# Performance work log

Hardware: AMD Instinct MI355X
Metric: run time of the kernel (lower is better)

## Reference

```python
import jax, jax.numpy as jnp
import numpy as np

D_MODEL = 1024
N_HEADS = 16
D_HEAD = D_MODEL // N_HEADS

def setup_inputs() -> dict:
    key = jax.random.key(0)
    k1, k2, k3 = jax.random.split(key, 3)
    x = jax.random.normal(k1, (4, 2048, D_MODEL), dtype=jnp.float32)
    # Linear weights stored as [in, out] for x @ W
    s = 1.0 / np.sqrt(D_MODEL)
    W_qkv = jax.random.uniform(k2, (D_MODEL, 3 * D_MODEL), jnp.float32, -s, s)
    W_out = jax.random.uniform(k3, (D_MODEL, D_MODEL), jnp.float32, -s, s)
    return {"x": x, "W_qkv": W_qkv, "W_out": W_out}

def reference(x, W_qkv, W_out):
    B, T, C = x.shape
    scale = D_HEAD ** -0.5
    qkv = x @ W_qkv                       # [B,T,3C]
    q, k, v = jnp.split(qkv, 3, axis=-1)
    def heads(t):
        return t.reshape(B, T, N_HEADS, D_HEAD).transpose(0, 2, 1, 3)  # [B,H,T,d]
    q, k, v = heads(q), heads(k), heads(v)
    att = jnp.einsum('bhqd,bhkd->bhqk', q, k) * scale  # [B,H,T,T]
    causal = jnp.tril(jnp.ones((T, T), dtype=bool))
    att = jnp.where(causal, att, -jnp.inf)
    att = jax.nn.softmax(att, axis=-1)
    y = jnp.einsum('bhqk,bhkd->bhqd', att, v)          # [B,H,T,d]
    y = y.transpose(0, 2, 1, 3).reshape(B, T, C)
    return y @ W_out
```

## Files before the change

kernel.cpp:

```cpp
#include <hip/hip_runtime.h>
#include <hip/hip_bf16.h>

typedef unsigned short u16;
typedef __attribute__((ext_vector_type(8))) short short8v;
typedef __attribute__((ext_vector_type(4))) float f32x4;
typedef __attribute__((ext_vector_type(16))) float f32x16;

#define Bb 4
#define Tt 2048
#define Cc 1024
#define Hh 16
#define C3 3072
#define Mm 8192

__device__ __forceinline__ u16 f2bf(float f) {
    union { __hip_bfloat16 h; u16 u; } r;
    r.h = __float2bfloat16(f);
    return r.u;
}
__device__ __forceinline__ unsigned int pk2(float a, float b) {
    union { __hip_bfloat162 h; unsigned int u; } r;
    r.h.x = __float2bfloat16(a);
    r.h.y = __float2bfloat16(b);
    return r.u;
}
__device__ __forceinline__ float exp2g(float x) {
#if __has_builtin(__builtin_amdgcn_exp2f)
    return __builtin_amdgcn_exp2f(x);
#else
    return exp2f(x);
#endif
}
__device__ __forceinline__ void plswap(unsigned int& a, unsigned int& b) {
#if __has_builtin(__builtin_amdgcn_permlane32_swap)
    typedef __attribute__((ext_vector_type(2))) unsigned int uint2v;
    uint2v r = __builtin_amdgcn_permlane32_swap(a, b, false, false);
    a = r.x; b = r.y;
#else
    asm volatile("v_permlane32_swap_b32 %0, %1" : "+v"(a), "+v"(b));
#endif
}
__device__ __forceinline__ void gload16(const void* g, void* l) {
    __builtin_amdgcn_global_load_lds(
        (const __attribute__((address_space(1))) unsigned int*)g,
        (__attribute__((address_space(3))) unsigned int*)l, 16, 0, 0);
}
__device__ __forceinline__ short8v scale8(short8v v, float s) {
    union { short8v sv; unsigned int u[4]; } in, out;
    in.sv = v;
#pragma unroll
    for (int i = 0; i < 4; ++i) {
        float lo = __uint_as_float(in.u[i] << 16);
        float hi = __uint_as_float(in.u[i] & 0xffff0000u);
        out.u[i] = pk2(lo * s, hi * s);
    }
    return out.sv;
}

__global__ __launch_bounds__(256) void cvt_x(const float* __restrict__ in,
                                             u16* __restrict__ out) {
    int i = blockIdx.x * 256 + threadIdx.x;
    float4 v = reinterpret_cast<const float4*>(in)[i];
    ushort4 o;
    o.x = f2bf(v.x); o.y = f2bf(v.y); o.z = f2bf(v.z); o.w = f2bf(v.w);
    reinterpret_cast<ushort4*>(out)[i] = o;
}

__global__ __launch_bounds__(256) void wtrans(const float* __restrict__ in,
                                              u16* __restrict__ out,
                                              int R, int Ccols) {
    __shared__ float t[32][33];
    const int tx = threadIdx.x & 31, ty = threadIdx.x >> 5;
    const int bx = blockIdx.x, by = blockIdx.y;
    const int c = bx * 32 + tx;
#pragma unroll
    for (int j = 0; j < 4; ++j) {
        int r = by * 32 + ty + j * 8;
        t[ty + j * 8][tx] = in[(size_t)r * Ccols + c];
    }
    __syncthreads();
#pragma unroll
    for (int j = 0; j < 4; ++j) {
        int orow = bx * 32 + ty + j * 8;
        int oc   = by * 32 + tx;
        out[(size_t)orow * R + oc] = f2bf(t[tx][ty + j * 8]);
    }
}

template <int OUTF32>
__global__ __launch_bounds__(256) void gemm_mfma(const u16* __restrict__ A,
                                                 const u16* __restrict__ BT,
                                                 void* __restrict__ C0,
                                                 int M, int N, int K) {
    __shared__ u16 As[128 * 32];
    __shared__ u16 Bs[128 * 32];
    const int tid = threadIdx.x;
    const int w = tid >> 6, l = tid & 63;
    const int wr = w >> 1, wc = w & 1;
    const int g = l >> 4, q = l & 15;
    const int bm = blockIdx.x * 128, bn = blockIdx.y * 128;
    const int lrow = l >> 2;
    const int lcol = (l & 3) * 8;

    f32x4 acc[4][4] = {};
    const u16* Ap = A + (size_t)(bm + w * 32 + lrow) * K + lcol;
    const u16* Bp = BT + (size_t)(bn + w * 32 + lrow) * K + lcol;

    for (int k0 = 0; k0 < K; k0 += 32) {
        gload16(Ap + k0, &As[(w * 32) * 32]);
        gload16(Ap + (size_t)16 * K + k0, &As[(w * 32 + 16) * 32]);
        gload16(Bp + k0, &Bs[(w * 32) * 32]);
        gload16(Bp + (size_t)16 * K + k0, &Bs[(w * 32 + 16) * 32]);
        __syncthreads();
        short8v af[4], bf[4];
#pragma unroll
        for (int m = 0; m < 4; ++m)
            af[m] = *reinterpret_cast<const short8v*>(&As[(wr * 64 + m * 16 + q) * 32 + g * 8]);
#pragma unroll
        for (int n = 0; n < 4; ++n)
            bf[n] = *reinterpret_cast<const short8v*>(&Bs[(wc * 64 + n * 16 + q) * 32 + g * 8]);
#pragma unroll
        for (int m = 0; m < 4; ++m)
#pragma unroll
            for (int n = 0; n < 4; ++n)
                acc[m][n] = __builtin_amdgcn_mfma_f32_16x16x32_bf16(af[m], bf[n], acc[m][n], 0, 0, 0);
        __syncthreads();
    }

#pragma unroll
    for (int m = 0; m < 4; ++m)
#pragma unroll
        for (int n = 0; n < 4; ++n)
#pragma unroll
            for (int r = 0; r < 4; ++r) {
                int row = bm + wr * 64 + m * 16 + g * 4 + r;
                int col = bn + wc * 64 + n * 16 + q;
                if (OUTF32)
                    reinterpret_cast<float*>(C0)[(size_t)row * N + col] = acc[m][n][r];
                else
                    reinterpret_cast<u16*>(C0)[(size_t)row * N + col] = f2bf(acc[m][n][r]);
            }
}

__global__ __launch_bounds__(512, 2) void gemm256_qkv(const u16* __restrict__ A,
                                                      const u16* __restrict__ BT,
                                                      u16* __restrict__ qkOut,
                                                      u16* __restrict__ vTOut,
                                                      int K) {
    __shared__ u16 SM[65536];
    const int tid = threadIdx.x;
    const int wv = tid >> 6, L = tid & 63;
    const int wm = wv >> 2, wn = wv & 3;
    const int q = L & 15, g = L >> 4;
    const int bm = blockIdx.x * 256, bn = blockIdx.y * 256;
    const int nK = K >> 6;

    char* smB = (char*)SM;
    const int srow = wv * 16 + (L >> 3);
    const int scol = ((L & 7) ^ ((L >> 3) & 7)) * 8;
    const u16* Asrc = A + (size_t)(bm + srow) * K + scol;
    const u16* Bsrc = BT + (size_t)(bn + srow) * K + scol;

#define STG2(src, ldsByte)                                                \
    { gload16((src), smB + (ldsByte) + wv * 2048);                        \
      gload16((src) + 8 * (size_t)K, smB + (ldsByte) + wv * 2048 + 1024); }

    STG2(Asrc, 0)
    STG2(Asrc + 128 * (size_t)K, 16384)
    STG2(Bsrc, 32768)
    STG2(Bsrc + 128 * (size_t)K, 49152)
    STG2(Asrc + 64, 65536)
    STG2(Asrc + 128 * (size_t)K + 64, 65536 + 16384)
    STG2(Bsrc + 64, 65536 + 32768)

    const int rA = (wm * 128 + q) * 64;
    const int rB = 16384 + (wn * 64 + q) * 64;
    const int s0 = (g ^ (q & 7)) * 8;
    const int s1 = ((4 + g) ^ (q & 7)) * 8;

    f32x4 acc[8][4] = {};

#define LDA2(dst, mf)                                                                   \
    dst[0] = *reinterpret_cast<const short8v*>(&SM[bufU + rA + mf * 1024 + s0]);        \
    dst[1] = *reinterpret_cast<const short8v*>(&SM[bufU + rA + mf * 1024 + s1]);
#define LDB2(nf)                                                                        \
    Bf##nf[0] = *reinterpret_cast<const short8v*>(&SM[bufU + rB + nf * 1024 + s0]);     \
    Bf##nf[1] = *reinterpret_cast<const short8v*>(&SM[bufU + rB + nf * 1024 + s1]);
#define MMA2(Aa, nf, ia)                                                                       \
    acc[ia][nf] = __builtin_amdgcn_mfma_f32_16x16x32_bf16(Aa[0], Bf##nf[0], acc[ia][nf], 0, 0, 0); \
    acc[ia][nf] = __builtin_amdgcn_mfma_f32_16x16x32_bf16(Aa[1], Bf##nf[1], acc[ia][nf], 0, 0, 0);
#define MBLK2(Aa, Ab, ia, ib)                                             \
    __builtin_amdgcn_s_setprio(1);                                        \
    MMA2(Aa, 0, ia) MMA2(Aa, 1, ia) MMA2(Aa, 2, ia) MMA2(Aa, 3, ia)       \
    MMA2(Ab, 0, ib) MMA2(Ab, 1, ib) MMA2(Ab, 2, ib) MMA2(Ab, 3, ib)       \
    __builtin_amdgcn_s_setprio(0);

    for (int t = 0; t < nK; ++t) {
        const int bufU = (t & 1) * 32768;
        const int curB = (t & 1) * 65536;
        const int nxtB = ((t + 1) & 1) * 65536;
        if (t == nK - 1) { asm volatile("s_waitcnt vmcnt(0)" ::: "memory"); }
        else             { asm volatile("s_waitcnt vmcnt(6)" ::: "memory"); }
        __builtin_amdgcn_s_barrier();
        __builtin_amdgcn_sched_barrier(0);

        short8v Bf0[2], Bf1[2], Bf2[2], Bf3[2];
        LDB2(0) LDB2(1) LDB2(2) LDB2(3)
        short8v Af0[2], Af1[2];
        LDA2(Af0, 0) LDA2(Af1, 1)
        if (t + 1 < nK) STG2(Bsrc + 128 * (size_t)K + (t + 1) * 64, nxtB + 49152)
        __builtin_amdgcn_sched_barrier(0);
        MBLK2(Af0, Af1, 0, 1)
        __builtin_amdgcn_sched_barrier(0);

        short8v Af2[2], Af3[2];
        LDA2(Af2, 2) LDA2(Af3, 3)
        __builtin_amdgcn_sched_barrier(0);
        MBLK2(Af2, Af3, 2, 3)
        __builtin_amdgcn_sched_barrier(0);

        short8v Af4[2], Af5[2];
        LDA2(Af4, 4) LDA2(Af5, 5)
        __builtin_amdgcn_sched_barrier(0);
        MBLK2(Af4, Af5, 4, 5)
        __builtin_amdgcn_sched_barrier(0);

        short8v Af6[2], Af7[2];
        LDA2(Af6, 6) LDA2(Af7, 7)
        asm volatile("s_waitcnt lgkmcnt(0)" ::: "memory");
        __builtin_amdgcn_sched_barrier(0);
        __builtin_amdgcn_s_barrier();
        if (t + 2 < nK) {
            STG2(Asrc + (t + 2) * 64, curB)
            STG2(Asrc + 128 * (size_t)K + (t + 2) * 64, curB + 16384)
            STG2(Bsrc + (t + 2) * 64, curB + 32768)
        }
        __builtin_amdgcn_sched_barrier(0);
        MBLK2(Af6, Af7, 6, 7)
    }
#undef MMA2
#undef MBLK2
#undef LDA2
#undef LDB2
#undef STG2

    __builtin_amdgcn_s_barrier();
    if (bn < 2048) {
        char* smb2 = (char*)SM;
#pragma unroll
        for (int mf = 0; mf < 8; ++mf) {
            const int row = wm * 128 + mf * 16 + g * 4;
#pragma unroll
            for (int nf = 0; nf < 4; ++nf) {
                const int col = wn * 64 + nf * 16 + q;
#pragma unroll
                for (int rr = 0; rr < 4; ++rr) {
                    const int r2 = row + rr;
                    *(u16*)(smb2 + r2 * 512 + ((((col >> 3) ^ (r2 & 7))) << 4) + (col & 7) * 2)
                        = f2bf(acc[mf][nf][rr]);
                }
            }
        }
        __syncthreads();
        const int erow = tid >> 1;
        const int ebase = (tid & 1) * 16;
        u16* orow = qkOut + (size_t)(bm + erow) * 2048 + bn;
#pragma unroll
        for (int j = 0; j < 16; ++j) {
            const int s = ebase + j;
            uint4 v = *(const uint4*)(smb2 + erow * 512 + ((s ^ (erow & 7)) << 4));
            *reinterpret_cast<uint4*>(orow + s * 8) = v;
        }
    } else {
        const int colb = bn - 2048 + wn * 64;
        const int bI = bm >> 11;
        const int tIb = (bm & 2047) + wm * 128 + g * 4;
#pragma unroll
        for (int mf = 0; mf < 8; ++mf)
#pragma unroll
            for (int nf = 0; nf < 4; ++nf) {
                const int col = colb + nf * 16 + q;
                uint2 pv;
                pv.x = pk2(acc[mf][nf][0], acc[mf][nf][1]);
                pv.y = pk2(acc[mf][nf][2], acc[mf][nf][3]);
                *reinterpret_cast<uint2*>(
                    &vTOut[((size_t)bI * 1024 + col) * 2048 + tIb + mf * 16]) = pv;
            }
    }
}

__global__ __launch_bounds__(256) void attn_mfma(const u16* __restrict__ qk,
                                                 const u16* __restrict__ vT,
                                                 u16* __restrict__ y) {
    __shared__ u16 SM[9216];
    const int tid = threadIdx.x;
    const int w = tid >> 6, l = tid & 63;
    const int q31 = l & 31, hi = l >> 5;
    const int bid = blockIdx.x;
    const int bh = bid & 63;
    const int chunk = 15 - (bid >> 6);
    const int b = bh >> 4, h = bh & 15;
    const size_t tok0 = (size_t)b * Tt;

    const float C2 = 0.18033688011112042f;

    const int srow = tid >> 2;
    const int sseg = (tid & 3) * 16;
    const int soff = srow * 72 + sseg;
    const u16* gK = qk + (tok0 + srow) * 2048 + 1024 + h * 64 + sseg;
    const u16* gV = vT + ((size_t)b * 1024 + h * 64 + srow) * 2048 + sseg;

    const int nsteps = 2 * (chunk + 1);
    const int q0w = chunk * 128 + w * 32;
    const int qlane = q0w + q31;

    short8v qf0, qf1, qf2, qf3;
    {
        const u16* qp = qk + (tok0 + qlane) * 2048 + h * 64 + hi * 8;
        qf0 = scale8(*reinterpret_cast<const short8v*>(qp), C2);
        qf1 = scale8(*reinterpret_cast<const short8v*>(qp + 16), C2);
        qf2 = scale8(*reinterpret_cast<const short8v*>(qp + 32), C2);
        qf3 = scale8(*reinterpret_cast<const short8v*>(qp + 48), C2);
    }

    f32x16 acc0 = {}, acc1 = {};
    float l_run = 0.f;

    {
        uint4 ka = *reinterpret_cast<const uint4*>(gK);
        uint4 kb = *reinterpret_cast<const uint4*>(gK + 8);
        uint4 va = *reinterpret_cast<const uint4*>(gV);
        uint4 vb = *reinterpret_cast<const uint4*>(gV + 8);
        *reinterpret_cast<uint4*>(&SM[soff]) = ka;
        *reinterpret_cast<uint4*>(&SM[soff + 8]) = kb;
        *reinterpret_cast<uint4*>(&SM[4608 + soff]) = va;
        *reinterpret_cast<uint4*>(&SM[4608 + soff + 8]) = vb;
    }
    __syncthreads();

    for (int t = 0; t < nsteps; ++t) {
        const int k0 = t * 64;
        const bool pre = (t + 1 < nsteps);
        uint4 ka = {}, kb = {}, va = {}, vb = {};
        if (pre) {
            const u16* gKt = gK + (size_t)(t + 1) * 64 * 2048;
            const u16* gVt = gV + (t + 1) * 64;
            ka = *reinterpret_cast<const uint4*>(gKt);
            kb = *reinterpret_cast<const uint4*>(gKt + 8);
            va = *reinterpret_cast<const uint4*>(gVt);
            vb = *reinterpret_cast<const uint4*>(gVt + 8);
        }

        if (k0 <= q0w + 31) {
            const u16* Kb = SM;
            const u16* Vb = SM + 4608;
            f32x16 st0 = {}, st1 = {};
#pragma unroll
            for (int s = 0; s < 4; ++s) {
                short8v kfa = *reinterpret_cast<const short8v*>(&Kb[q31 * 72 + s * 16 + hi * 8]);
                short8v kfb = *reinterpret_cast<const short8v*>(&Kb[(q31 + 32) * 72 + s * 16 + hi * 8]);
                short8v qs = (s == 0) ? qf0 : (s == 1) ? qf1 : (s == 2) ? qf2 : qf3;
                st0 = __builtin_amdgcn_mfma_f32_32x32x16_bf16(kfa, qs, st0, 0, 0, 0);
                st1 = __builtin_amdgcn_mfma_f32_32x32x16_bf16(kfb, qs, st1, 0, 0, 0);
            }
            const bool diag = (k0 + 63 > q0w);
            float s0[16], s1[16];
            float rs = 0.f;
#pragma unroll
            for (int r = 0; r < 16; ++r) {
                int krel = (r & 3) + 8 * (r >> 2) + 4 * hi;
                float v0 = st0[r];
                float v1 = st1[r];
                if (diag) {
                    if (k0 + krel > qlane) v0 = -1e30f;
                    if (k0 + 32 + krel > qlane) v1 = -1e30f;
                }
                float p0 = exp2g(v0);
                float p1 = exp2g(v1);
                s0[r] = p0; s1[r] = p1;
                rs += p0 + p1;
            }
            rs += __shfl_xor(rs, 32);
            l_run += rs;

            short8v pf0, pf1, pf2, pf3;
#define MKFRAG(dst, P, rb)                                                  \
            {                                                               \
                unsigned int a_ = pk2(P[rb + 0], P[rb + 1]);                \
                unsigned int b_ = pk2(P[rb + 4], P[rb + 5]);                \
                unsigned int c_ = pk2(P[rb + 2], P[rb + 3]);                \
                unsigned int d_ = pk2(P[rb + 6], P[rb + 7]);                \
                plswap(a_, b_);                                             \
                plswap(c_, d_);                                             \
                union { unsigned int u[4]; short8v s; } uf_;                \
                uf_.u[0] = a_; uf_.u[1] = c_; uf_.u[2] = b_; uf_.u[3] = d_; \
                dst = uf_.s;                                                \
            }
            MKFRAG(pf0, s0, 0)
            MKFRAG(pf1, s0, 8)
            MKFRAG(pf2, s1, 0)
            MKFRAG(pf3, s1, 8)
#undef MKFRAG
#pragma unroll
            for (int s = 0; s < 4; ++s) {
                short8v vfa = *reinterpret_cast<const short8v*>(&Vb[q31 * 72 + s * 16 + hi * 8]);
                short8v vfb = *reinterpret_cast<const short8v*>(&Vb[(q31 + 32) * 72 + s * 16 + hi * 8]);
                short8v ps = (s == 0) ? pf0 : (s == 1) ? pf1 : (s == 2) ? pf2 : pf3;
                acc0 = __builtin_amdgcn_mfma_f32_32x32x16_bf16(vfa, ps, acc0, 0, 0, 0);
                acc1 = __builtin_amdgcn_mfma_f32_32x32x16_bf16(vfb, ps, acc1, 0, 0, 0);
            }
        }

        __syncthreads();
        if (pre) {
            *reinterpret_cast<uint4*>(&SM[soff]) = ka;
            *reinterpret_cast<uint4*>(&SM[soff + 8]) = kb;
            *reinterpret_cast<uint4*>(&SM[4608 + soff]) = va;
            *reinterpret_cast<uint4*>(&SM[4608 + soff + 8]) = vb;
        }
        __syncthreads();
    }

    const float inv = 1.f / l_run;
    unsigned int* Od2 = reinterpret_cast<unsigned int*>(SM);
    const int qrow = w * 32 + q31;
#pragma unroll
    for (int r = 0; r < 16; r += 2) {
        int d0 = (r & 3) + 8 * (r >> 2) + 4 * hi;
        Od2[qrow * 36 + (d0 >> 1)] = pk2(acc0[r] * inv, acc0[r + 1] * inv);
        Od2[qrow * 36 + ((32 + d0) >> 1)] = pk2(acc1[r] * inv, acc1[r + 1] * inv);
    }
    __syncthreads();
    {
        const int row = w * 32 + (l >> 1);
        const int dh = (l & 1) * 32;
        const u16* src = SM + row * 72 + dh;
        u16* dst = y + (tok0 + chunk * 128 + row) * Cc + h * 64 + dh;
#pragma unroll
        for (int k2 = 0; k2 < 4; ++k2)
            *reinterpret_cast<uint4*>(dst + k2 * 8) =
                *reinterpret_cast<const uint4*>(src + k2 * 8);
    }
}

extern "C" void kernel_launch(void* const* d_in, const int* in_sizes, int n_in,
                              void* d_out, int out_size, void* d_ws, size_t ws_size,
                              hipStream_t stream) {
    const float* x    = (const float*)d_in[0];
    const float* Wqkv = (const float*)d_in[1];
    const float* Wout = (const float*)d_in[2];
    float* out = (float*)d_out;

    char* ws = (char*)d_ws;
    u16* qk    = (u16*)(ws);
    u16* vT    = (u16*)(ws + 33554432);
    u16* xbf   = (u16*)(ws + 50331648);
    u16* WqkvT = (u16*)(ws + 67108864);
    u16* WoutT = (u16*)(ws + 73400320);

    cvt_x<<<(Mm * Cc) / (256 * 4), 256, 0, stream>>>(x, xbf);
    wtrans<<<dim3(C3 / 32, Cc / 32), 256, 0, stream>>>(Wqkv, WqkvT, Cc, C3);
    wtrans<<<dim3(Cc / 32, Cc / 32), 256, 0, stream>>>(Wout, WoutT, Cc, Cc);

    gemm256_qkv<<<dim3(Mm / 256, C3 / 256), 512, 0, stream>>>(xbf, WqkvT, qk, vT, Cc);

    u16* ybf = xbf;
    attn_mfma<<<1024, 256, 0, stream>>>(qk, vT, ybf);

    gemm_mfma<1><<<dim3(Mm / 128, Cc / 128), 256, 0, stream>>>(ybf, WoutT, out, Mm, Cc, Cc);
}
```

Baseline: 180.9 us.

## Replace double-buffered async QKV GEMM pipeline with single-buffer synchronous loads

Halves the QKV GEMM's shared memory from 128KB to 64KB by dropping the double-buffered, prefetch-ahead global-to-LDS pipeline. Each K-step now loads its tile, synchronizes, computes, and synchronizes again. The epilogue stages the bf16 output in two 128-row halves so it fits the smaller buffer. The likely aim is higher occupancy (two blocks per CU under launch_bounds 512,2), but load latency is no longer overlapped with MFMA work and the hand-tuned scheduling barriers are removed.

```diff
diff --git a/kernel.cpp b/kernel.cpp
--- a/kernel.cpp
+++ b/kernel.cpp
@@ -147,7 +147,7 @@
                                                       u16* __restrict__ qkOut,
                                                       u16* __restrict__ vTOut,
                                                       int K) {
-    __shared__ u16 SM[65536];
+    __shared__ u16 SM[32768];
     const int tid = threadIdx.x;
     const int wv = tid >> 6, L = tid & 63;
     const int wm = wv >> 2, wn = wv & 3;
@@ -165,14 +165,6 @@
     { gload16((src), smB + (ldsByte) + wv * 2048);                        \
       gload16((src) + 8 * (size_t)K, smB + (ldsByte) + wv * 2048 + 1024); }
 
-    STG2(Asrc, 0)
-    STG2(Asrc + 128 * (size_t)K, 16384)
-    STG2(Bsrc, 32768)
-    STG2(Bsrc + 128 * (size_t)K, 49152)
-    STG2(Asrc + 64, 65536)
-    STG2(Asrc + 128 * (size_t)K + 64, 65536 + 16384)
-    STG2(Bsrc + 64, 65536 + 32768)
-
     const int rA = (wm * 128 + q) * 64;
     const int rB = 16384 + (wn * 64 + q) * 64;
     const int s0 = (g ^ (q & 7)) * 8;
@@ -180,12 +172,12 @@
 
     f32x4 acc[8][4] = {};
 
-#define LDA2(dst, mf)                                                                   \
-    dst[0] = *reinterpret_cast<const short8v*>(&SM[bufU + rA + mf * 1024 + s0]);        \
-    dst[1] = *reinterpret_cast<const short8v*>(&SM[bufU + rA + mf * 1024 + s1]);
-#define LDB2(nf)                                                                        \
-    Bf##nf[0] = *reinterpret_cast<const short8v*>(&SM[bufU + rB + nf * 1024 + s0]);     \
-    Bf##nf[1] = *reinterpret_cast<const short8v*>(&SM[bufU + rB + nf * 1024 + s1]);
+#define LDA2(dst, mf)                                                              \
+    dst[0] = *reinterpret_cast<const short8v*>(&SM[rA + mf * 1024 + s0]);          \
+    dst[1] = *reinterpret_cast<const short8v*>(&SM[rA + mf * 1024 + s1]);
+#define LDB2(nf)                                                                   \
+    Bf##nf[0] = *reinterpret_cast<const short8v*>(&SM[rB + nf * 1024 + s0]);       \
+    Bf##nf[1] = *reinterpret_cast<const short8v*>(&SM[rB + nf * 1024 + s1]);
 #define MMA2(Aa, nf, ia)                                                                       \
     acc[ia][nf] = __builtin_amdgcn_mfma_f32_16x16x32_bf16(Aa[0], Bf##nf[0], acc[ia][nf], 0, 0, 0); \
     acc[ia][nf] = __builtin_amdgcn_mfma_f32_16x16x32_bf16(Aa[1], Bf##nf[1], acc[ia][nf], 0, 0, 0);
@@ -196,47 +188,27 @@
     __builtin_amdgcn_s_setprio(0);
 
     for (int t = 0; t < nK; ++t) {
-        const int bufU = (t & 1) * 32768;
-        const int curB = (t & 1) * 65536;
-        const int nxtB = ((t + 1) & 1) * 65536;
-        if (t == nK - 1) { asm volatile("s_waitcnt vmcnt(0)" ::: "memory"); }
-        else             { asm volatile("s_waitcnt vmcnt(6)" ::: "memory"); }
-        __builtin_amdgcn_s_barrier();
-        __builtin_amdgcn_sched_barrier(0);
+        STG2(Asrc + t * 64, 0)
+        STG2(Asrc + 128 * (size_t)K + t * 64, 16384)
+        STG2(Bsrc + t * 64, 32768)
+        STG2(Bsrc + 128 * (size_t)K + t * 64, 49152)
+        __syncthreads();
 
         short8v Bf0[2], Bf1[2], Bf2[2], Bf3[2];
         LDB2(0) LDB2(1) LDB2(2) LDB2(3)
         short8v Af0[2], Af1[2];
         LDA2(Af0, 0) LDA2(Af1, 1)
-        if (t + 1 < nK) STG2(Bsrc + 128 * (size_t)K + (t + 1) * 64, nxtB + 49152)
-        __builtin_amdgcn_sched_barrier(0);
         MBLK2(Af0, Af1, 0, 1)
-        __builtin_amdgcn_sched_barrier(0);
-
         short8v Af2[2], Af3[2];
         LDA2(Af2, 2) LDA2(Af3, 3)
-        __builtin_amdgcn_sched_barrier(0);
         MBLK2(Af2, Af3, 2, 3)
-        __builtin_amdgcn_sched_barrier(0);
-
         short8v Af4[2], Af5[2];
         LDA2(Af4, 4) LDA2(Af5, 5)
-        __builtin_amdgcn_sched_barrier(0);
         MBLK2(Af4, Af5, 4, 5)
-        __builtin_amdgcn_sched_barrier(0);
-
         short8v Af6[2], Af7[2];
         LDA2(Af6, 6) LDA2(Af7, 7)
-        asm volatile("s_waitcnt lgkmcnt(0)" ::: "memory");
-        __builtin_amdgcn_sched_barrier(0);
-        __builtin_amdgcn_s_barrier();
-        if (t + 2 < nK) {
-            STG2(Asrc + (t + 2) * 64, curB)
-            STG2(Asrc + 128 * (size_t)K + (t + 2) * 64, curB + 16384)
-            STG2(Bsrc + (t + 2) * 64, curB + 32768)
-        }
-        __builtin_amdgcn_sched_barrier(0);
         MBLK2(Af6, Af7, 6, 7)
+        __syncthreads();
     }
 #undef MMA2
 #undef MBLK2
@@ -244,32 +216,39 @@
 #undef LDB2
 #undef STG2
 
-    __builtin_amdgcn_s_barrier();
     if (bn < 2048) {
         char* smb2 = (char*)SM;
 #pragma unroll
-        for (int mf = 0; mf < 8; ++mf) {
-            const int row = wm * 128 + mf * 16 + g * 4;
-#pragma unroll
-            for (int nf = 0; nf < 4; ++nf) {
-                const int col = wn * 64 + nf * 16 + q;
-#pragma unroll
-                for (int rr = 0; rr < 4; ++rr) {
-                    const int r2 = row + rr;
-                    *(u16*)(smb2 + r2 * 512 + ((((col >> 3) ^ (r2 & 7))) << 4) + (col & 7) * 2)
-                        = f2bf(acc[mf][nf][rr]);
+        for (int p = 0; p < 2; ++p) {
+            if (wm == p) {
+#pragma unroll
+                for (int mf = 0; mf < 8; ++mf) {
+                    const int lr0 = mf * 16 + g * 4;
+#pragma unroll
+                    for (int nf = 0; nf < 4; ++nf) {
+                        const int col = wn * 64 + nf * 16 + q;
+#pragma unroll
+                        for (int rr = 0; rr < 4; ++rr) {
+                            const int lr = lr0 + rr;
+                            *(u16*)(smb2 + lr * 512 + ((((col >> 3) ^ (lr & 7))) << 4) + (col & 7) * 2)
+                                = f2bf(acc[mf][nf][rr]);
+                        }
+                    }
                 }
             }
-        }
-        __syncthreads();
-        const int erow = tid >> 1;
-        const int ebase = (tid & 1) * 16;
-        u16* orow = qkOut + (size_t)(bm + erow) * 2048 + bn;
-#pragma unroll
-        for (int j = 0; j < 16; ++j) {
-            const int s = ebase + j;
-            uint4 v = *(const uint4*)(smb2 + erow * 512 + ((s ^ (erow & 7)) << 4));
-            *reinterpret_cast<uint4*>(orow + s * 8) = v;
+            __syncthreads();
+            {
+                const int row_ = tid >> 2;
+                const int sb = (tid & 3) * 8;
+                u16* orow = qkOut + (size_t)(bm + p * 128 + row_) * 2048 + bn;
+#pragma unroll
+                for (int j = 0; j < 8; ++j) {
+                    const int s = sb + j;
+                    uint4 v = *(const uint4*)(smb2 + row_ * 512 + ((s ^ (row_ & 7)) << 4));
+                    *reinterpret_cast<uint4*>(orow + s * 8) = v;
+                }
+            }
+            __syncthreads();
         }
     } else {
         const int colb = bn - 2048 + wn * 64;
```

Measured after the change: 193.2 us. 1.07x slower.
